# Kernel tuning notes

Hardware: AMD Instinct MI355X
Metric: run time of the kernel (lower is better)

Reference implementation:

```python
import jax, jax.numpy as jnp
import numpy as np

D_MODEL = 1024
NUM_HEADS = 16
HEAD_DIM = D_MODEL // NUM_HEADS
B, S = 2, 2048


def setup_inputs() -> dict:
    key = jax.random.key(0)
    ks = jax.random.split(key, 6)
    scale = 0.02
    return {
        "x": jax.random.normal(ks[0], (B, S, D_MODEL), dtype=jnp.float32),
        "mask": jax.random.normal(ks[1], (S, S), dtype=jnp.float32),
        "Wqkv": jax.random.normal(ks[2], (D_MODEL, 3 * D_MODEL), dtype=jnp.float32) * scale,
        "bqkv": jax.random.normal(ks[3], (3 * D_MODEL,), dtype=jnp.float32) * scale,
        "Wout": jax.random.normal(ks[4], (D_MODEL, D_MODEL), dtype=jnp.float32) * scale,
        "bout": jax.random.normal(ks[5], (D_MODEL,), dtype=jnp.float32) * scale,
    }


def reference(x, mask, Wqkv, bqkv, Wout, bout):
    b, s, d = x.shape
    h, hd = NUM_HEADS, HEAD_DIM
    qkv = x @ Wqkv + bqkv                              # [b, s, 3d]
    qkv = qkv.reshape(b, s, h, 3 * hd).transpose(0, 2, 1, 3)  # [b, h, s, 3hd]
    q, k, v = jnp.split(qkv, 3, axis=-1)               # each [b, h, s, hd]
    scaled = jnp.einsum("bhqd,bhkd->bhqk", q, k) / jnp.sqrt(jnp.float32(hd))
    scaled = scaled + mask                             # mask [s, s] broadcasts
    attn = jax.nn.softmax(scaled, axis=-1)
    values = jnp.einsum("bhqk,bhkd->bhqd", attn, v)    # [b, h, s, hd]
    values = values.transpose(0, 2, 1, 3).reshape(b, s, d)
    return values @ Wout + bout
```

## Files before the change

kernel.cpp:

```cpp
#include <hip/hip_runtime.h>
#include <hip/hip_bf16.h>

#define D_MODEL 1024
#define NH 16
#define HD 64
#define BATCH 2
#define SEQ 2048
#define M_TOTAL (BATCH*SEQ)

typedef _Float16 f16;
typedef _Float16 half8 __attribute__((ext_vector_type(8)));
typedef _Float16 half4v __attribute__((ext_vector_type(4)));
typedef float floatx4 __attribute__((ext_vector_type(4)));

__device__ inline void gload_lds16(const void* g, void* l) {
    __builtin_amdgcn_global_load_lds(
        (const __attribute__((address_space(1))) unsigned int*)g,
        (__attribute__((address_space(3))) unsigned int*)l, 16, 0, 0);
}

__global__ void cvt_f32_f16(const float* __restrict__ src, f16* __restrict__ dst, int n4) {
    int i = blockIdx.x * blockDim.x + threadIdx.x;
    if (i < n4) {
        const float4* s = (const float4*)src;
        float4 v = s[i];
        half4v o = { (f16)v.x, (f16)v.y, (f16)v.z, (f16)v.w };
        *(half4v*)(dst + (long)i * 4) = o;
    }
}

__global__ void transpose_cvt(const float* __restrict__ src, f16* __restrict__ dst, int R, int C) {
    __shared__ float tile[32][33];
    int tx = threadIdx.x;
    int ty = threadIdx.y;
    int c0 = blockIdx.x * 32;
    int r0 = blockIdx.y * 32;
    for (int yy = 0; yy < 32; yy += 8)
        tile[ty + yy][tx] = src[(long)(r0 + ty + yy) * C + c0 + tx];
    __syncthreads();
    for (int yy = 0; yy < 32; yy += 8)
        dst[(long)(c0 + ty + yy) * R + r0 + tx] = (f16)tile[tx][ty + yy];
}

__global__ void mask_rowmax(const float* __restrict__ mask, float* __restrict__ mm) {
    int row = blockIdx.x;
    const float* r = mask + (long)row * SEQ;
    float m = -3e38f;
    for (int i = threadIdx.x; i < SEQ; i += 256) m = fmaxf(m, r[i]);
    for (int off = 1; off < 64; off <<= 1) m = fmaxf(m, __shfl_xor(m, off));
    __shared__ float red[4];
    if ((threadIdx.x & 63) == 0) red[threadIdx.x >> 6] = m;
    __syncthreads();
    if (threadIdx.x == 0)
        mm[row] = fmaxf(fmaxf(red[0], red[1]), fmaxf(red[2], red[3]));
}

template<int MODE>
__global__ __launch_bounds__(256) void gemm128(
    const f16* __restrict__ A, const f16* __restrict__ BT,
    const float* __restrict__ bias,
    f16* __restrict__ Qh, f16* __restrict__ Kh, f16* __restrict__ Vtg,
    float* __restrict__ out, int Kdim)
{
    __shared__ f16 Ah[128 * 32];
    __shared__ f16 Bh[128 * 32];
    int tid  = threadIdx.x;
    int wid  = tid >> 6;
    int lane = tid & 63;
    int quad = lane >> 4;
    int l16  = lane & 15;
    int m0 = blockIdx.y * 128;
    int n0 = blockIdx.x * 128;
    int srow = lane >> 2;
    int scol = (lane & 3) * 8;
    int mrow = (wid >> 1) * 64;
    int ncol = (wid & 1) * 64;

    floatx4 acc[4][4];
    #pragma unroll
    for (int mb = 0; mb < 4; mb++)
        #pragma unroll
        for (int nb = 0; nb < 4; nb++) acc[mb][nb] = (floatx4){0.f, 0.f, 0.f, 0.f};

    const f16* Abase = A + (long)m0 * Kdim;
    const f16* Bbase = BT + (long)n0 * Kdim;

    for (int k0 = 0; k0 < Kdim; k0 += 32) {
        #pragma unroll
        for (int j = 0; j < 2; j++) {
            int rbase = (wid * 2 + j) * 16;
            gload_lds16(Abase + (long)(rbase + srow) * Kdim + k0 + scol, &Ah[rbase * 32]);
            gload_lds16(Bbase + (long)(rbase + srow) * Kdim + k0 + scol, &Bh[rbase * 32]);
        }
        __syncthreads();
        half8 af[4];
        #pragma unroll
        for (int mb = 0; mb < 4; mb++)
            af[mb] = *(const half8*)&Ah[(mrow + mb * 16 + l16) * 32 + quad * 8];
        #pragma unroll
        for (int nb = 0; nb < 4; nb++) {
            half8 bf = *(const half8*)&Bh[(ncol + nb * 16 + l16) * 32 + quad * 8];
            #pragma unroll
            for (int mb = 0; mb < 4; mb++)
                acc[mb][nb] = __builtin_amdgcn_mfma_f32_16x16x32_f16(af[mb], bf, acc[mb][nb], 0, 0, 0);
        }
        __syncthreads();
    }

    #pragma unroll
    for (int nb = 0; nb < 4; nb++) {
        int n = n0 + ncol + nb * 16 + l16;
        float bv = bias[n];
        int head = 0, t = 0, d = 0;
        if (MODE == 0) { head = n / 192; int rem = n % 192; t = rem / 64; d = rem % 64; }
        #pragma unroll
        for (int mb = 0; mb < 4; mb++) {
            int mbase = m0 + mrow + mb * 16 + quad * 4;
            if (MODE == 0) {
                int b = mbase >> 11;
                int s = mbase & 2047;
                long bh = b * NH + head;
                if (t == 2) {
                    half4v pack;
                    #pragma unroll
                    for (int r = 0; r < 4; r++) pack[r] = (f16)(acc[mb][nb][r] + bv);
                    *(half4v*)&Vtg[(bh * HD + d) * SEQ + s] = pack;
                } else if (t == 0) {
                    #pragma unroll
                    for (int r = 0; r < 4; r++)
                        Qh[(bh * SEQ + s + r) * HD + d] = (f16)((acc[mb][nb][r] + bv) * 0.125f);
                } else {
                    #pragma unroll
                    for (int r = 0; r < 4; r++)
                        Kh[(bh * SEQ + s + r) * HD + d] = (f16)(acc[mb][nb][r] + bv);
                }
            } else {
                #pragma unroll
                for (int r = 0; r < 4; r++)
                    out[(long)(mbase + r) * D_MODEL + n] = acc[mb][nb][r] + bv;
            }
        }
    }
}

__global__ __launch_bounds__(256, 4) void attn(
    const f16* __restrict__ Qh, const f16* __restrict__ Kh, const f16* __restrict__ Vtg,
    const float* __restrict__ mask, const float* __restrict__ mm, f16* __restrict__ valh)
{
    __shared__ f16 Kl[64 * 72];
    __shared__ f16 Vt[64 * 72];
    __shared__ f16 Pl[4][16 * 68];
    int tid  = threadIdx.x;
    int wid  = tid >> 6;
    int lane = tid & 63;
    int quad = lane >> 4;
    int l16  = lane & 15;
    int bh = blockIdx.y;
    int b  = bh >> 4;
    int h  = bh & 15;
    int q0 = blockIdx.x * 64 + wid * 16;

    const f16* Qbase = Qh + ((long)bh * SEQ + q0) * HD;
    half8 qf0 = *(const half8*)&Qbase[(long)l16 * HD + quad * 8];
    half8 qf1 = *(const half8*)&Qbase[(long)l16 * HD + 32 + quad * 8];

    float mml[4];
    #pragma unroll
    for (int r = 0; r < 4; r++) mml[r] = mm[q0 + quad * 4 + r];

    floatx4 Of[4];
    float sums[4] = {0.f, 0.f, 0.f, 0.f};
    #pragma unroll
    for (int nb = 0; nb < 4; nb++) Of[nb] = (floatx4){0.f, 0.f, 0.f, 0.f};

    int srow = tid >> 2;
    int scg  = (tid & 3) * 16;
    const f16* Kb = Kh + (long)bh * SEQ * HD;
    const f16* Vb = Vtg + (long)bh * HD * SEQ;

    for (int k0 = 0; k0 < SEQ; k0 += 64) {
        __syncthreads();
        *(half8*)&Kl[srow * 72 + scg]     = *(const half8*)&Kb[(long)(k0 + srow) * HD + scg];
        *(half8*)&Kl[srow * 72 + scg + 8] = *(const half8*)&Kb[(long)(k0 + srow) * HD + scg + 8];
        *(half8*)&Vt[srow * 72 + scg]     = *(const half8*)&Vb[(long)srow * SEQ + k0 + scg];
        *(half8*)&Vt[srow * 72 + scg + 8] = *(const half8*)&Vb[(long)srow * SEQ + k0 + scg + 8];
        __syncthreads();

        floatx4 sc[4];
        #pragma unroll
        for (int kb = 0; kb < 4; kb++) {
            half8 kf0 = *(const half8*)&Kl[(kb * 16 + l16) * 72 + quad * 8];
            half8 kf1 = *(const half8*)&Kl[(kb * 16 + l16) * 72 + 32 + quad * 8];
            floatx4 s = (floatx4){0.f, 0.f, 0.f, 0.f};
            s = __builtin_amdgcn_mfma_f32_16x16x32_f16(qf0, kf0, s, 0, 0, 0);
            s = __builtin_amdgcn_mfma_f32_16x16x32_f16(qf1, kf1, s, 0, 0, 0);
            sc[kb] = s;
        }

        #pragma unroll
        for (int kb = 0; kb < 4; kb++) {
            int colg = k0 + kb * 16 + l16;
            #pragma unroll
            for (int r = 0; r < 4; r++) {
                float sv = sc[kb][r] + mask[(long)(q0 + quad * 4 + r) * SEQ + colg];
                float p = __expf(sv - mml[r]);
                sums[r] += p;
                Pl[wid][(quad * 4 + r) * 68 + kb * 16 + l16] = (f16)p;
            }
        }

        half8 pf0 = *(const half8*)&Pl[wid][l16 * 68 + quad * 8];
        half8 pf1 = *(const half8*)&Pl[wid][l16 * 68 + 32 + quad * 8];
        #pragma unroll
        for (int nb = 0; nb < 4; nb++) {
            half8 vf0 = *(const half8*)&Vt[(nb * 16 + l16) * 72 + quad * 8];
            half8 vf1 = *(const half8*)&Vt[(nb * 16 + l16) * 72 + 32 + quad * 8];
            Of[nb] = __builtin_amdgcn_mfma_f32_16x16x32_f16(pf0, vf0, Of[nb], 0, 0, 0);
            Of[nb] = __builtin_amdgcn_mfma_f32_16x16x32_f16(pf1, vf1, Of[nb], 0, 0, 0);
        }
    }

    #pragma unroll
    for (int r = 0; r < 4; r++) {
        float s = sums[r];
        s += __shfl_xor(s, 1);
        s += __shfl_xor(s, 2);
        s += __shfl_xor(s, 4);
        s += __shfl_xor(s, 8);
        sums[r] = 1.f / s;
    }

    #pragma unroll
    for (int nb = 0; nb < 4; nb++) {
        #pragma unroll
        for (int r = 0; r < 4; r++) {
            int q = q0 + quad * 4 + r;
            int d = nb * 16 + l16;
            valh[((long)(b * SEQ + q)) * D_MODEL + h * HD + d] = (f16)(Of[nb][r] * sums[r]);
        }
    }
}

extern "C" void kernel_launch(void* const* d_in, const int* in_sizes, int n_in,
                              void* d_out, int out_size, void* d_ws, size_t ws_size,
                              hipStream_t stream) {
    const float* x    = (const float*)d_in[0];
    const float* mask = (const float*)d_in[1];
    const float* Wqkv = (const float*)d_in[2];
    const float* bqkv = (const float*)d_in[3];
    const float* Wout = (const float*)d_in[4];
    const float* bout = (const float*)d_in[5];
    float* out = (float*)d_out;

    char* ws = (char*)d_ws;
    f16* xh    = (f16*)(ws + 0);
    f16* WqkvT = (f16*)(ws + 8388608);
    f16* WoutT = (f16*)(ws + 14680064);
    f16* Qh    = (f16*)(ws + 16777216);
    f16* Kh    = (f16*)(ws + 25165824);
    f16* Vtg   = (f16*)(ws + 33554432);
    f16* valh  = (f16*)(ws + 41943040);
    float* mmax = (float*)(ws + 50331648);

    cvt_f32_f16<<<4096, 256, 0, stream>>>(x, xh, M_TOTAL * D_MODEL / 4);
    transpose_cvt<<<dim3(96, 32), dim3(32, 8), 0, stream>>>(Wqkv, WqkvT, 1024, 3072);
    transpose_cvt<<<dim3(32, 32), dim3(32, 8), 0, stream>>>(Wout, WoutT, 1024, 1024);
    mask_rowmax<<<2048, 256, 0, stream>>>(mask, mmax);
    gemm128<0><<<dim3(24, 32), 256, 0, stream>>>(xh, WqkvT, bqkv, Qh, Kh, Vtg, nullptr, 1024);
    attn<<<dim3(32, 32), 256, 0, stream>>>(Qh, Kh, Vtg, mask, mmax, valh);
    gemm128<1><<<dim3(8, 32), 256, 0, stream>>>(valh, WoutT, bout, nullptr, nullptr, nullptr, out, 1024);
}
```

Measured before the change: 246.6 us.

## Precompute exp(mask) in fp16, widen attention tiles, swizzle LDS in GEMMs

Replaces the mask row-max pass with an exp(mask) fp16 table, so attention computes p = exp(mask)*exp(qk) without a max subtraction. The table reuses the xh workspace slot after the QKV GEMM, and attention reads half-size fp16 mask data. Attention blocks now handle 32 query rows per wave, raising K/V reuse, and load K/V through async global-to-LDS copies with an XOR swizzle. The GEMMs move to a K step of 64 with a swizzled LDS layout, and the output projection uses 64-wide N tiles to launch more blocks. This drops max-based numerical safety: exp of the raw scores and mask can overflow fp16 or fp32 for larger inputs.

```diff
diff --git a/kernel.cpp b/kernel.cpp
--- a/kernel.cpp
+++ b/kernel.cpp
@@ -22,9 +22,17 @@
 __global__ void cvt_f32_f16(const float* __restrict__ src, f16* __restrict__ dst, int n4) {
     int i = blockIdx.x * blockDim.x + threadIdx.x;
     if (i < n4) {
-        const float4* s = (const float4*)src;
-        float4 v = s[i];
+        float4 v = ((const float4*)src)[i];
         half4v o = { (f16)v.x, (f16)v.y, (f16)v.z, (f16)v.w };
+        *(half4v*)(dst + (long)i * 4) = o;
+    }
+}
+
+__global__ void exp_cvt(const float* __restrict__ src, f16* __restrict__ dst, int n4) {
+    int i = blockIdx.x * blockDim.x + threadIdx.x;
+    if (i < n4) {
+        float4 v = ((const float4*)src)[i];
+        half4v o = { (f16)__expf(v.x), (f16)__expf(v.y), (f16)__expf(v.z), (f16)__expf(v.w) };
         *(half4v*)(dst + (long)i * 4) = o;
     }
 }
@@ -42,73 +50,71 @@
         dst[(long)(c0 + ty + yy) * R + r0 + tx] = (f16)tile[tx][ty + yy];
 }
 
-__global__ void mask_rowmax(const float* __restrict__ mask, float* __restrict__ mm) {
-    int row = blockIdx.x;
-    const float* r = mask + (long)row * SEQ;
-    float m = -3e38f;
-    for (int i = threadIdx.x; i < SEQ; i += 256) m = fmaxf(m, r[i]);
-    for (int off = 1; off < 64; off <<= 1) m = fmaxf(m, __shfl_xor(m, off));
-    __shared__ float red[4];
-    if ((threadIdx.x & 63) == 0) red[threadIdx.x >> 6] = m;
-    __syncthreads();
-    if (threadIdx.x == 0)
-        mm[row] = fmaxf(fmaxf(red[0], red[1]), fmaxf(red[2], red[3]));
-}
-
-template<int MODE>
-__global__ __launch_bounds__(256) void gemm128(
+template<int MODE, int TN>
+__global__ __launch_bounds__(256) void gemm_mfma(
     const f16* __restrict__ A, const f16* __restrict__ BT,
     const float* __restrict__ bias,
     f16* __restrict__ Qh, f16* __restrict__ Kh, f16* __restrict__ Vtg,
     float* __restrict__ out, int Kdim)
 {
-    __shared__ f16 Ah[128 * 32];
-    __shared__ f16 Bh[128 * 32];
+    constexpr int NF = TN / 32;
+    __shared__ f16 Ah[128 * 64];
+    __shared__ f16 Bh[TN * 64];
     int tid  = threadIdx.x;
     int wid  = tid >> 6;
     int lane = tid & 63;
     int quad = lane >> 4;
     int l16  = lane & 15;
     int m0 = blockIdx.y * 128;
-    int n0 = blockIdx.x * 128;
-    int srow = lane >> 2;
-    int scol = (lane & 3) * 8;
+    int n0 = blockIdx.x * TN;
     int mrow = (wid >> 1) * 64;
-    int ncol = (wid & 1) * 64;
-
-    floatx4 acc[4][4];
+    int ncol = (wid & 1) * (TN / 2);
+    int grow = lane >> 3;
+    int gchunk = (lane & 7) ^ (grow & 7);
+    int sw0 = ((quad)     ^ (l16 & 7)) * 8;
+    int sw1 = ((quad + 4) ^ (l16 & 7)) * 8;
+
+    floatx4 acc[4][NF];
     #pragma unroll
     for (int mb = 0; mb < 4; mb++)
         #pragma unroll
-        for (int nb = 0; nb < 4; nb++) acc[mb][nb] = (floatx4){0.f, 0.f, 0.f, 0.f};
+        for (int nb = 0; nb < NF; nb++) acc[mb][nb] = (floatx4){0.f, 0.f, 0.f, 0.f};
 
     const f16* Abase = A + (long)m0 * Kdim;
     const f16* Bbase = BT + (long)n0 * Kdim;
 
-    for (int k0 = 0; k0 < Kdim; k0 += 32) {
-        #pragma unroll
-        for (int j = 0; j < 2; j++) {
-            int rbase = (wid * 2 + j) * 16;
-            gload_lds16(Abase + (long)(rbase + srow) * Kdim + k0 + scol, &Ah[rbase * 32]);
-            gload_lds16(Bbase + (long)(rbase + srow) * Kdim + k0 + scol, &Bh[rbase * 32]);
+    for (int k0 = 0; k0 < Kdim; k0 += 64) {
+        #pragma unroll
+        for (int j = 0; j < 4; j++) {
+            int r = j * 32 + wid * 8 + grow;
+            gload_lds16(Abase + (long)r * Kdim + k0 + gchunk * 8, &Ah[(j * 32 + wid * 8) * 64]);
+        }
+        #pragma unroll
+        for (int j = 0; j < TN / 32; j++) {
+            int r = j * 32 + wid * 8 + grow;
+            gload_lds16(Bbase + (long)r * Kdim + k0 + gchunk * 8, &Bh[(j * 32 + wid * 8) * 64]);
         }
         __syncthreads();
-        half8 af[4];
-        #pragma unroll
-        for (int mb = 0; mb < 4; mb++)
-            af[mb] = *(const half8*)&Ah[(mrow + mb * 16 + l16) * 32 + quad * 8];
-        #pragma unroll
-        for (int nb = 0; nb < 4; nb++) {
-            half8 bf = *(const half8*)&Bh[(ncol + nb * 16 + l16) * 32 + quad * 8];
+        #pragma unroll
+        for (int h = 0; h < 2; h++) {
+            int sw = h ? sw1 : sw0;
+            half8 af[4];
             #pragma unroll
             for (int mb = 0; mb < 4; mb++)
-                acc[mb][nb] = __builtin_amdgcn_mfma_f32_16x16x32_f16(af[mb], bf, acc[mb][nb], 0, 0, 0);
+                af[mb] = *(const half8*)&Ah[(mrow + mb * 16 + l16) * 64 + sw];
+            #pragma unroll
+            for (int nb = 0; nb < NF; nb++) {
+                half8 bf = *(const half8*)&Bh[(ncol + nb * 16 + l16) * 64 + sw];
+                #pragma unroll
+                for (int mb = 0; mb < 4; mb++)
+                    acc[mb][nb] = __builtin_amdgcn_mfma_f32_16x16x32_f16(af[mb], bf, acc[mb][nb], 0, 0, 0);
+            }
         }
         __syncthreads();
     }
 
     #pragma unroll
-    for (int nb = 0; nb < 4; nb++) {
+    for (int nb = 0; nb < NF; nb++) {
         int n = n0 + ncol + nb * 16 + l16;
         float bv = bias[n];
         int head = 0, t = 0, d = 0;
@@ -143,13 +149,13 @@
     }
 }
 
-__global__ __launch_bounds__(256, 4) void attn(
+__global__ __launch_bounds__(256) void attn(
     const f16* __restrict__ Qh, const f16* __restrict__ Kh, const f16* __restrict__ Vtg,
-    const float* __restrict__ mask, const float* __restrict__ mm, f16* __restrict__ valh)
+    const f16* __restrict__ E, f16* __restrict__ valh)
 {
-    __shared__ f16 Kl[64 * 72];
-    __shared__ f16 Vt[64 * 72];
-    __shared__ f16 Pl[4][16 * 68];
+    __shared__ f16 Kl[64 * 64];
+    __shared__ f16 Vt[64 * 64];
+    __shared__ f16 Pl[4][32 * 68];
     int tid  = threadIdx.x;
     int wid  = tid >> 6;
     int lane = tid & 63;
@@ -158,87 +164,120 @@
     int bh = blockIdx.y;
     int b  = bh >> 4;
     int h  = bh & 15;
-    int q0 = blockIdx.x * 64 + wid * 16;
+    int q0 = blockIdx.x * 128 + wid * 32;
+
+    int grow = lane >> 3;
+    int gchunk = (lane & 7) ^ (grow & 7);
+    int sw0 = ((quad)     ^ (l16 & 7)) * 8;
+    int sw1 = ((quad + 4) ^ (l16 & 7)) * 8;
 
     const f16* Qbase = Qh + ((long)bh * SEQ + q0) * HD;
-    half8 qf0 = *(const half8*)&Qbase[(long)l16 * HD + quad * 8];
-    half8 qf1 = *(const half8*)&Qbase[(long)l16 * HD + 32 + quad * 8];
-
-    float mml[4];
-    #pragma unroll
-    for (int r = 0; r < 4; r++) mml[r] = mm[q0 + quad * 4 + r];
-
-    floatx4 Of[4];
-    float sums[4] = {0.f, 0.f, 0.f, 0.f};
-    #pragma unroll
-    for (int nb = 0; nb < 4; nb++) Of[nb] = (floatx4){0.f, 0.f, 0.f, 0.f};
-
-    int srow = tid >> 2;
-    int scg  = (tid & 3) * 16;
+    half8 qf[2][2];
+    #pragma unroll
+    for (int m = 0; m < 2; m++)
+        #pragma unroll
+        for (int c = 0; c < 2; c++)
+            qf[m][c] = *(const half8*)&Qbase[(long)(m * 16 + l16) * HD + c * 32 + quad * 8];
+
+    floatx4 Of[2][4];
+    float sums[2][4];
+    #pragma unroll
+    for (int m = 0; m < 2; m++) {
+        #pragma unroll
+        for (int nb = 0; nb < 4; nb++) Of[m][nb] = (floatx4){0.f, 0.f, 0.f, 0.f};
+        #pragma unroll
+        for (int r = 0; r < 4; r++) sums[m][r] = 0.f;
+    }
+
     const f16* Kb = Kh + (long)bh * SEQ * HD;
     const f16* Vb = Vtg + (long)bh * HD * SEQ;
 
     for (int k0 = 0; k0 < SEQ; k0 += 64) {
         __syncthreads();
-        *(half8*)&Kl[srow * 72 + scg]     = *(const half8*)&Kb[(long)(k0 + srow) * HD + scg];
-        *(half8*)&Kl[srow * 72 + scg + 8] = *(const half8*)&Kb[(long)(k0 + srow) * HD + scg + 8];
-        *(half8*)&Vt[srow * 72 + scg]     = *(const half8*)&Vb[(long)srow * SEQ + k0 + scg];
-        *(half8*)&Vt[srow * 72 + scg + 8] = *(const half8*)&Vb[(long)srow * SEQ + k0 + scg + 8];
+        #pragma unroll
+        for (int j = 0; j < 2; j++) {
+            int r = j * 32 + wid * 8 + grow;
+            gload_lds16(Kb + (long)(k0 + r) * HD + gchunk * 8, &Kl[(j * 32 + wid * 8) * 64]);
+            gload_lds16(Vb + (long)r * SEQ + k0 + gchunk * 8, &Vt[(j * 32 + wid * 8) * 64]);
+        }
         __syncthreads();
 
-        floatx4 sc[4];
+        f16 ef[2][4][4];
+        #pragma unroll
+        for (int m = 0; m < 2; m++)
+            #pragma unroll
+            for (int r = 0; r < 4; r++) {
+                const f16* Erow = E + (long)(q0 + m * 16 + quad * 4 + r) * SEQ + k0 + l16;
+                #pragma unroll
+                for (int kb = 0; kb < 4; kb++) ef[m][r][kb] = Erow[kb * 16];
+            }
+
+        floatx4 sc[2][4];
         #pragma unroll
         for (int kb = 0; kb < 4; kb++) {
-            half8 kf0 = *(const half8*)&Kl[(kb * 16 + l16) * 72 + quad * 8];
-            half8 kf1 = *(const half8*)&Kl[(kb * 16 + l16) * 72 + 32 + quad * 8];
-            floatx4 s = (floatx4){0.f, 0.f, 0.f, 0.f};
-            s = __builtin_amdgcn_mfma_f32_16x16x32_f16(qf0, kf0, s, 0, 0, 0);
-            s = __builtin_amdgcn_mfma_f32_16x16x32_f16(qf1, kf1, s, 0, 0, 0);
-            sc[kb] = s;
-        }
-
-        #pragma unroll
-        for (int kb = 0; kb < 4; kb++) {
-            int colg = k0 + kb * 16 + l16;
+            half8 kf0 = *(const half8*)&Kl[(kb * 16 + l16) * 64 + sw0];
+            half8 kf1 = *(const half8*)&Kl[(kb * 16 + l16) * 64 + sw1];
+            #pragma unroll
+            for (int m = 0; m < 2; m++) {
+                floatx4 s = (floatx4){0.f, 0.f, 0.f, 0.f};
+                s = __builtin_amdgcn_mfma_f32_16x16x32_f16(qf[m][0], kf0, s, 0, 0, 0);
+                s = __builtin_amdgcn_mfma_f32_16x16x32_f16(qf[m][1], kf1, s, 0, 0, 0);
+                sc[m][kb] = s;
+            }
+        }
+
+        #pragma unroll
+        for (int m = 0; m < 2; m++)
+            #pragma unroll
+            for (int kb = 0; kb < 4; kb++)
+                #pragma unroll
+                for (int r = 0; r < 4; r++) {
+                    float p = (float)ef[m][r][kb] * __expf(sc[m][kb][r]);
+                    sums[m][r] += p;
+                    Pl[wid][(m * 16 + quad * 4 + r) * 68 + kb * 16 + l16] = (f16)p;
+                }
+
+        half8 pf[2][2];
+        #pragma unroll
+        for (int m = 0; m < 2; m++)
+            #pragma unroll
+            for (int c = 0; c < 2; c++)
+                pf[m][c] = *(const half8*)&Pl[wid][(m * 16 + l16) * 68 + c * 32 + quad * 8];
+
+        #pragma unroll
+        for (int nb = 0; nb < 4; nb++) {
+            half8 vf0 = *(const half8*)&Vt[(nb * 16 + l16) * 64 + sw0];
+            half8 vf1 = *(const half8*)&Vt[(nb * 16 + l16) * 64 + sw1];
+            #pragma unroll
+            for (int m = 0; m < 2; m++) {
+                Of[m][nb] = __builtin_amdgcn_mfma_f32_16x16x32_f16(pf[m][0], vf0, Of[m][nb], 0, 0, 0);
+                Of[m][nb] = __builtin_amdgcn_mfma_f32_16x16x32_f16(pf[m][1], vf1, Of[m][nb], 0, 0, 0);
+            }
+        }
+    }
+
+    #pragma unroll
+    for (int m = 0; m < 2; m++)
+        #pragma unroll
+        for (int r = 0; r < 4; r++) {
+            float s = sums[m][r];
+            s += __shfl_xor(s, 1);
+            s += __shfl_xor(s, 2);
+            s += __shfl_xor(s, 4);
+            s += __shfl_xor(s, 8);
+            sums[m][r] = 1.f / s;
+        }
+
+    #pragma unroll
+    for (int m = 0; m < 2; m++)
+        #pragma unroll
+        for (int nb = 0; nb < 4; nb++)
             #pragma unroll
             for (int r = 0; r < 4; r++) {
-                float sv = sc[kb][r] + mask[(long)(q0 + quad * 4 + r) * SEQ + colg];
-                float p = __expf(sv - mml[r]);
-                sums[r] += p;
-                Pl[wid][(quad * 4 + r) * 68 + kb * 16 + l16] = (f16)p;
-            }
-        }
-
-        half8 pf0 = *(const half8*)&Pl[wid][l16 * 68 + quad * 8];
-        half8 pf1 = *(const half8*)&Pl[wid][l16 * 68 + 32 + quad * 8];
-        #pragma unroll
-        for (int nb = 0; nb < 4; nb++) {
-            half8 vf0 = *(const half8*)&Vt[(nb * 16 + l16) * 72 + quad * 8];
-            half8 vf1 = *(const half8*)&Vt[(nb * 16 + l16) * 72 + 32 + quad * 8];
-            Of[nb] = __builtin_amdgcn_mfma_f32_16x16x32_f16(pf0, vf0, Of[nb], 0, 0, 0);
-            Of[nb] = __builtin_amdgcn_mfma_f32_16x16x32_f16(pf1, vf1, Of[nb], 0, 0, 0);
-        }
-    }
-
-    #pragma unroll
-    for (int r = 0; r < 4; r++) {
-        float s = sums[r];
-        s += __shfl_xor(s, 1);
-        s += __shfl_xor(s, 2);
-        s += __shfl_xor(s, 4);
-        s += __shfl_xor(s, 8);
-        sums[r] = 1.f / s;
-    }
-
-    #pragma unroll
-    for (int nb = 0; nb < 4; nb++) {
-        #pragma unroll
-        for (int r = 0; r < 4; r++) {
-            int q = q0 + quad * 4 + r;
-            int d = nb * 16 + l16;
-            valh[((long)(b * SEQ + q)) * D_MODEL + h * HD + d] = (f16)(Of[nb][r] * sums[r]);
-        }
-    }
+                int q = q0 + m * 16 + quad * 4 + r;
+                int d = nb * 16 + l16;
+                valh[((long)(b * SEQ + q)) * D_MODEL + h * HD + d] = (f16)(Of[m][nb][r] * sums[m][r]);
+            }
 }
 
 extern "C" void kernel_launch(void* const* d_in, const int* in_sizes, int n_in,
@@ -254,19 +293,19 @@
 
     char* ws = (char*)d_ws;
     f16* xh    = (f16*)(ws + 0);
+    f16* E     = (f16*)(ws + 0);
     f16* WqkvT = (f16*)(ws + 8388608);
     f16* WoutT = (f16*)(ws + 14680064);
     f16* Qh    = (f16*)(ws + 16777216);
     f16* Kh    = (f16*)(ws + 25165824);
     f16* Vtg   = (f16*)(ws + 33554432);
     f16* valh  = (f16*)(ws + 41943040);
-    float* mmax = (float*)(ws + 50331648);
 
     cvt_f32_f16<<<4096, 256, 0, stream>>>(x, xh, M_TOTAL * D_MODEL / 4);
     transpose_cvt<<<dim3(96, 32), dim3(32, 8), 0, stream>>>(Wqkv, WqkvT, 1024, 3072);
     transpose_cvt<<<dim3(32, 32), dim3(32, 8), 0, stream>>>(Wout, WoutT, 1024, 1024);
-    mask_rowmax<<<2048, 256, 0, stream>>>(mask, mmax);
-    gemm128<0><<<dim3(24, 32), 256, 0, stream>>>(xh, WqkvT, bqkv, Qh, Kh, Vtg, nullptr, 1024);
-    attn<<<dim3(32, 32), 256, 0, stream>>>(Qh, Kh, Vtg, mask, mmax, valh);
-    gemm128<1><<<dim3(8, 32), 256, 0, stream>>>(valh, WoutT, bout, nullptr, nullptr, nullptr, out, 1024);
-}
+    gemm_mfma<0, 128><<<dim3(24, 32), 256, 0, stream>>>(xh, WqkvT, bqkv, Qh, Kh, Vtg, nullptr, 1024);
+    exp_cvt<<<4096, 256, 0, stream>>>(mask, E, SEQ * SEQ / 4);
+    attn<<<dim3(16, 32), 256, 0, stream>>>(Qh, Kh, Vtg, E, valh);
+    gemm_mfma<1, 64><<<dim3(16, 32), 256, 0, stream>>>(valh, WoutT, bout, nullptr, nullptr, nullptr, out, 1024);
+}
```

Result: faster. 229.7 us (-6.9%).
